# Kernel tuning notes

Measured on AMD Instinct MI355X. Metric: run time of the kernel, lower is better.

The kernel has to match this reference:

```python
import jax, jax.numpy as jnp
import numpy as np

B, CIN, N, K, G, COUT = 8, 128, 2048, 16, 4, 256
NL = COUT // 4          # nl_channels = int(0.25*out_channels) = 64
L = COUT - NL           # l_channels = 192
CL = L // G             # 48 per local head
CNL = NL // G           # 16 per non-local head


def setup_inputs() -> dict:
    key = jax.random.key(0)
    ks = jax.random.split(key, 16)
    s = 0.05
    r = lambda k_, sh: s * jax.random.normal(k_, sh, jnp.float32)
    return {
        "x": jax.random.normal(ks[0], (B, CIN, N, K), jnp.float32),
        "abs_x": jax.random.normal(ks[1], (B, CIN // 2, N, 1), jnp.float32),
        "points": jax.random.normal(ks[2], (B, 3, N), jnp.float32),
        "Wq": r(ks[3], (L, CIN // 2)),
        "Wk": r(ks[4], (L, CIN // 2)),
        "Wv": r(ks[5], (L, CIN)),
        "Wnq": r(ks[6], (NL, CIN // 2)),
        "Wnk": r(ks[7], (NL, CIN // 2)),
        "Wnv1": r(ks[8], (NL, CIN // 2)),
        "Wnv2": r(ks[9], (NL, CIN // 2)),
        "pe_w1": r(ks[10], (3, L)),
        "pe_b1": jnp.zeros((L,), jnp.float32),
        "pe_w2": r(ks[11], (L, L)),
        "pe_b2": jnp.zeros((L,), jnp.float32),
        "npe_w1": r(ks[12], (G, 3, CNL)),
        "npe_b1": jnp.zeros((G, CNL), jnp.float32),
        "npe_w2": r(ks[13], (G, CNL, CNL)),
        "npe_b2": jnp.zeros((G, CNL), jnp.float32),
        "idx": jax.random.randint(ks[14], (B, 1, N, K), 0, N, dtype=jnp.int32),
    }


def _forward(x, abs_x, points, Wq, Wk, Wv, Wnq, Wnk, Wnv1, Wnv2,
             pe_w1, pe_b1, pe_w2, pe_b2, npe_w1, npe_b1, npe_w2, npe_b2, idx):
    b, c, n, k = x.shape
    half = c // 2
    idx_sq = idx[:, 0]                                   # (b,n,k)

    # ---- 1. Local attention over kNN neighbors ----
    lq = jnp.einsum('oc,bcns->bons', Wq, abs_x).reshape(b, G, CL, n, 1)
    lk = jnp.einsum('oc,bcnk->bonk', Wk, x[:, half:] + x[:, :half]).reshape(b, G, CL, n, k)
    lv = jnp.einsum('oc,bcnk->bonk', Wv, x).reshape(b, G, CL, n, k)

    # absolute positional encoding (select_neighbors -> carte MLP)
    nbr = jax.vmap(lambda p, i: p[:, i])(points, idx_sq)  # (b,3,n,k)
    rel = nbr - nbr[..., 0:1]                             # subtract first neighbor
    h = jax.nn.relu(jnp.einsum('bcnk,cd->bnkd', rel, pe_w1) + pe_b1)
    pe = (jnp.einsum('bnkd,de->bnke', h, pe_w2) + pe_b2).transpose(0, 3, 1, 2)
    lk = lk + pe.reshape(b, G, CL, n, k)

    att = jax.nn.softmax((lq * lk).sum(2), axis=-1)       # (b,G,n,k)
    local_feature = jnp.einsum('bgnk,bgcnk->bgcn', att, lv).reshape(b, L, n, 1)

    # ---- scatter-based sparse attention centrality + top-k node selection ----
    idx_flat = idx_sq.reshape(b, n * k)
    att_flat = att.reshape(b, G, n * k)

    def scat(a_g, i):  # a_g: (G, n*k), i: (n*k,)
        return jax.vmap(lambda a: jnp.zeros((n,), a.dtype).at[i].add(a))(a_g)

    cent = jax.vmap(scat)(att_flat, idx_flat)             # (b,G,n)
    vals, inds = jax.lax.top_k(cent, k)                   # (b,G,k)

    # ---- 2. Non-local MHA over selected nodes ----
    a2 = abs_x[..., 0]                                    # (b,half,n)
    nq = jnp.einsum('oc,bcn->bon', Wnq, a2).reshape(b, G, CNL, n)
    nk_ = jnp.einsum('oc,bcn->bon', Wnk, a2).reshape(b, G, CNL, n)
    nv1 = jnp.einsum('oc,bcn->bon', Wnv1, a2).reshape(b, G, CNL, n)
    nv2 = jnp.einsum('oc,bcn->bon', Wnv2, a2).reshape(b, G, CNL, n)

    gi = inds[:, :, None, :]                              # (b,G,1,k)
    nk_sel = jnp.take_along_axis(nk_, gi, axis=3)         # (b,G,CNL,k)
    nv2j = jnp.take_along_axis(nv2, gi, axis=3)           # (b,G,CNL,k)

    # per-group non-local positional encoding (constant over n by construction)
    sel = jnp.take_along_axis(jnp.broadcast_to(points[:, None], (b, G, 3, n)), gi, axis=3)  # (b,G,3,k)
    rel_nl = sel - sel[..., 0:1]
    h2 = jax.nn.relu(jnp.einsum('bgck,gcd->bgkd', rel_nl, npe_w1) + npe_b1[None, :, None, :])
    pe_nl = (jnp.einsum('bgkd,gde->bgke', h2, npe_w2) + npe_b2[None, :, None, :]).transpose(0, 1, 3, 2)  # (b,G,CNL,k)

    att_nl = jax.nn.softmax(jnp.einsum('bgcn,bgck->bgnk', nq, nk_sel + pe_nl), axis=-1)
    # value[b,g,c,n,k] = nv1[...,n] - nv2[...,n] + nv2j[...,k], gated by tanh(centrality)
    w = att_nl * jnp.tanh(vals)[:, :, None, :]            # (b,G,n,k)
    s = w.sum(-1)                                         # (b,G,n)
    nl_feature = (nv1 - nv2) * s[:, :, None, :] + jnp.einsum('bgnk,bgck->bgcn', w, nv2j)
    nl_feature = nl_feature.reshape(b, NL, n, 1)

    return jnp.concatenate([local_feature, nl_feature], axis=1)  # (b,COUT,n,1)


def reference(x, abs_x, points, Wq, Wk, Wv, Wnq, Wnk, Wnv1, Wnv2,
              pe_w1, pe_b1, pe_w2, pe_b2, npe_w1, npe_b1, npe_w2, npe_b2, idx):
    return _forward(x, abs_x, points, Wq, Wk, Wv, Wnq, Wnk, Wnv1, Wnv2,
                    pe_w1, pe_b1, pe_w2, pe_b2, npe_w1, npe_b1, npe_w2, npe_b2, idx)
```

## Files before the change

kernel.cpp:

```cpp
#include <hip/hip_runtime.h>
#include <cstddef>

constexpr int NN = 2048;
constexpr int GG = 4;

__global__ __launch_bounds__(256) void prep_q(const float* __restrict__ Wq,
                                              const float* __restrict__ Wk,
                                              const float* __restrict__ pe_w2,
                                              float* __restrict__ Qbuf) {
    const int g = blockIdx.x >> 6, c2 = blockIdx.x & 63;
    const int row = threadIdx.x;
    float acc = 0.f;
    if (row < 64) {
        for (int j = 0; j < 48; ++j) {
            const int o = g * 48 + j;
            acc = fmaf(Wk[o * 64 + row], Wq[o * 64 + c2], acc);
        }
    } else {
        const int d = row - 64;
        for (int j = 0; j < 48; ++j) {
            const int o = g * 48 + j;
            acc = fmaf(pe_w2[(size_t)d * 192 + o], Wq[o * 64 + c2], acc);
        }
    }
    Qbuf[((size_t)(g * 64 + c2) << 8) + row] = acc;
}

__global__ __launch_bounds__(256, 3) void local_v8(
    const float* __restrict__ x, const float* __restrict__ abs_x,
    const float* __restrict__ points, const float* __restrict__ Wv,
    const float* __restrict__ pe_w1, const float* __restrict__ pe_b1,
    const int* __restrict__ idx, const float* __restrict__ Qbuf,
    float* __restrict__ out, float* __restrict__ cent)
{
    const int bn = blockIdx.x;
    const int b  = bn >> 8;
    const int n0 = (bn & 255) << 3;
    const int tid = threadIdx.x;

    __shared__ int   sidx[128];
    __shared__ float sa2[64][8];
    __shared__ __align__(16) float s_big[4224];
    __shared__ float spart[128][9];
    __shared__ float s_small[544];

    float* sq   = s_big;
    float* sw2  = s_big;
    float* sxw  = s_big;
    float* spts = s_small;
    float* satt = s_small;

    if (tid < 128) sidx[tid] = idx[((size_t)b * NN + n0) * 16 + tid];
    for (int i = tid; i < 512; i += 256) {
        int c = i >> 3, nl = i & 7;
        sa2[c][nl] = abs_x[((size_t)b * 64 + c) * NN + n0 + nl];
    }
    __syncthreads();

    for (int i = tid; i < 384; i += 256) {
        int c3 = i >> 7, r = i & 127;
        spts[(c3 * 8 + (r >> 4)) * 16 + (r & 15)] =
            points[((size_t)b * 3 + c3) * NN + sidx[r]];
    }
    {
        const int g = tid >> 6, row = tid & 63;
        const float* qb = Qbuf + (((size_t)g * 64) << 8) + row;
        float a0 = 0.f, a1 = 0.f, a2v = 0.f, a3 = 0.f,
              a4 = 0.f, a5 = 0.f, a6 = 0.f, a7 = 0.f;
        for (int c2 = 0; c2 < 64; c2 += 8) {
            float qv[8];
            #pragma unroll
            for (int j = 0; j < 8; ++j) qv[j] = qb[(c2 + j) << 8];
            #pragma unroll
            for (int j = 0; j < 8; ++j) {
                const float4 v0 = *(const float4*)&sa2[c2 + j][0];
                const float4 v1 = *(const float4*)&sa2[c2 + j][4];
                a0 = fmaf(qv[j], v0.x, a0); a1 = fmaf(qv[j], v0.y, a1);
                a2v = fmaf(qv[j], v0.z, a2v); a3 = fmaf(qv[j], v0.w, a3);
                a4 = fmaf(qv[j], v1.x, a4); a5 = fmaf(qv[j], v1.y, a5);
                a6 = fmaf(qv[j], v1.z, a6); a7 = fmaf(qv[j], v1.w, a7);
            }
        }
        const int base = (g << 3) * 65 + row;
        sq[base + 0 * 65] = a0; sq[base + 1 * 65] = a1;
        sq[base + 2 * 65] = a2v; sq[base + 3 * 65] = a3;
        sq[base + 4 * 65] = a4; sq[base + 5 * 65] = a5;
        sq[base + 6 * 65] = a6; sq[base + 7 * 65] = a7;
    }
    __syncthreads();

    const int col = tid & 127, dh = tid >> 7;
    const int nlc = col >> 4, kkc = col & 15;

    {
        const float* xp = x + (((size_t)(b * 128 + dh * 32) * NN) + n0 + nlc) * 16 + kkc;
        const size_t cstr = (size_t)NN * 16;
        const float* q0 = &sq[((0 << 3) + nlc) * 65 + dh * 32];
        const float* q1 = &sq[((1 << 3) + nlc) * 65 + dh * 32];
        const float* q2 = &sq[((2 << 3) + nlc) * 65 + dh * 32];
        const float* q3 = &sq[((3 << 3) + nlc) * 65 + dh * 32];
        float a0 = 0.f, a1 = 0.f, a2v = 0.f, a3 = 0.f;
        for (int i0 = 0; i0 < 32; i0 += 8) {
            float lo[8], hi[8];
            #pragma unroll
            for (int j = 0; j < 8; ++j) {
                lo[j] = xp[(size_t)(i0 + j) * cstr];
                hi[j] = xp[(size_t)(i0 + j + 64) * cstr];
            }
            #pragma unroll
            for (int j = 0; j < 8; ++j) {
                const float xs = lo[j] + hi[j];
                a0 = fmaf(q0[i0 + j], xs, a0);
                a1 = fmaf(q1[i0 + j], xs, a1);
                a2v = fmaf(q2[i0 + j], xs, a2v);
                a3 = fmaf(q3[i0 + j], xs, a3);
            }
        }
        spart[col][dh * 4 + 0] = a0; spart[col][dh * 4 + 1] = a1;
        spart[col][dh * 4 + 2] = a2v; spart[col][dh * 4 + 3] = a3;
    }

    float4 xpre[16];
    #pragma unroll
    for (int t = 0; t < 4; ++t) {
        const int i2 = t * 256 + tid;
        const int c = i2 >> 3, nl = i2 & 7;
        const float* xp4 = x + (((size_t)(b * 128 + c) * NN) + n0 + nl) * 16;
        xpre[t * 4 + 0] = *(const float4*)(xp4);
        xpre[t * 4 + 1] = *(const float4*)(xp4 + 4);
        xpre[t * 4 + 2] = *(const float4*)(xp4 + 8);
        xpre[t * 4 + 3] = *(const float4*)(xp4 + 12);
    }
    __syncthreads();

    const float r0 = spts[(0 * 8 + nlc) * 16 + kkc] - spts[(0 * 8 + nlc) * 16];
    const float r1 = spts[(1 * 8 + nlc) * 16 + kkc] - spts[(1 * 8 + nlc) * 16];
    const float r2 = spts[(2 * 8 + nlc) * 16 + kkc] - spts[(2 * 8 + nlc) * 16];
    #pragma unroll
    for (int p = 0; p < 2; ++p) {
        if (tid < 192) {
            const int d = tid;
            float w00=0.f,w01=0.f,w02=0.f,w03=0.f,w04=0.f,w05=0.f,w06=0.f,w07=0.f;
            float w10=0.f,w11=0.f,w12=0.f,w13=0.f,w14=0.f,w15=0.f,w16=0.f,w17=0.f;
            const float* qb0 = Qbuf + (((size_t)(2 * p + 0) * 64) << 8) + 64 + d;
            const float* qb1 = Qbuf + (((size_t)(2 * p + 1) * 64) << 8) + 64 + d;
            for (int c2 = 0; c2 < 64; c2 += 4) {
                float qv0[4], qv1[4];
                #pragma unroll
                for (int j = 0; j < 4; ++j) {
                    qv0[j] = qb0[(c2 + j) << 8];
                    qv1[j] = qb1[(c2 + j) << 8];
                }
                #pragma unroll
                for (int j = 0; j < 4; ++j) {
                    const float4 v0 = *(const float4*)&sa2[c2 + j][0];
                    const float4 v1 = *(const float4*)&sa2[c2 + j][4];
                    w00 = fmaf(qv0[j], v0.x, w00); w01 = fmaf(qv0[j], v0.y, w01);
                    w02 = fmaf(qv0[j], v0.z, w02); w03 = fmaf(qv0[j], v0.w, w03);
                    w04 = fmaf(qv0[j], v1.x, w04); w05 = fmaf(qv0[j], v1.y, w05);
                    w06 = fmaf(qv0[j], v1.z, w06); w07 = fmaf(qv0[j], v1.w, w07);
                    w10 = fmaf(qv1[j], v0.x, w10); w11 = fmaf(qv1[j], v0.y, w11);
                    w12 = fmaf(qv1[j], v0.z, w12); w13 = fmaf(qv1[j], v0.w, w13);
                    w14 = fmaf(qv1[j], v1.x, w14); w15 = fmaf(qv1[j], v1.y, w15);
                    w16 = fmaf(qv1[j], v1.z, w16); w17 = fmaf(qv1[j], v1.w, w17);
                }
            }
            sw2[(0 * 8 + 0) * 196 + d] = w00; sw2[(0 * 8 + 1) * 196 + d] = w01;
            sw2[(0 * 8 + 2) * 196 + d] = w02; sw2[(0 * 8 + 3) * 196 + d] = w03;
            sw2[(0 * 8 + 4) * 196 + d] = w04; sw2[(0 * 8 + 5) * 196 + d] = w05;
            sw2[(0 * 8 + 6) * 196 + d] = w06; sw2[(0 * 8 + 7) * 196 + d] = w07;
            sw2[(1 * 8 + 0) * 196 + d] = w10; sw2[(1 * 8 + 1) * 196 + d] = w11;
            sw2[(1 * 8 + 2) * 196 + d] = w12; sw2[(1 * 8 + 3) * 196 + d] = w13;
            sw2[(1 * 8 + 4) * 196 + d] = w14; sw2[(1 * 8 + 5) * 196 + d] = w15;
            sw2[(1 * 8 + 6) * 196 + d] = w16; sw2[(1 * 8 + 7) * 196 + d] = w17;
        }
        __syncthreads();
        {
            float pB0 = 0.f, pB1 = 0.f;
            const float* w0 = &sw2[(0 * 8 + nlc) * 196];
            const float* w1 = &sw2[(1 * 8 + nlc) * 196];
            const int d0 = dh * 96;
            #pragma unroll 2
            for (int d = d0; d < d0 + 96; d += 4) {
                const float4 w1a = *(const float4*)&pe_w1[d];
                const float4 w1b = *(const float4*)&pe_w1[192 + d];
                const float4 w1c = *(const float4*)&pe_w1[384 + d];
                const float4 bb  = *(const float4*)&pe_b1[d];
                const float h0 = fmaxf(fmaf(r0, w1a.x, fmaf(r1, w1b.x, fmaf(r2, w1c.x, bb.x))), 0.f);
                const float h1 = fmaxf(fmaf(r0, w1a.y, fmaf(r1, w1b.y, fmaf(r2, w1c.y, bb.y))), 0.f);
                const float h2 = fmaxf(fmaf(r0, w1a.z, fmaf(r1, w1b.z, fmaf(r2, w1c.z, bb.z))), 0.f);
                const float h3 = fmaxf(fmaf(r0, w1a.w, fmaf(r1, w1b.w, fmaf(r2, w1c.w, bb.w))), 0.f);
                const float4 wa = *(const float4*)&w0[d];
                const float4 wb = *(const float4*)&w1[d];
                pB0 = fmaf(h0, wa.x, fmaf(h1, wa.y, fmaf(h2, wa.z, fmaf(h3, wa.w, pB0))));
                pB1 = fmaf(h0, wb.x, fmaf(h1, wb.y, fmaf(h2, wb.z, fmaf(h3, wb.w, pB1))));
            }
            spart[col][dh * 4 + 2 * p + 0] += pB0;
            spart[col][dh * 4 + 2 * p + 1] += pB1;
        }
        __syncthreads();
    }

    if (tid < 32) {
        const int g = tid >> 3, nl = tid & 7;
        float lg[16], m = -1e30f;
        #pragma unroll
        for (int kk = 0; kk < 16; ++kk) {
            const int cc = nl * 16 + kk;
            lg[kk] = spart[cc][g] + spart[cc][4 + g];
            m = fmaxf(m, lg[kk]);
        }
        float s = 0.f;
        #pragma unroll
        for (int kk = 0; kk < 16; ++kk) { lg[kk] = __expf(lg[kk] - m); s += lg[kk]; }
        const float inv = 1.f / s;
        #pragma unroll
        for (int kk = 0; kk < 16; ++kk) satt[nl * 68 + g * 16 + kk] = lg[kk] * inv;
    }
    __syncthreads();

    #pragma unroll
    for (int t = 0; t < 4; ++t) {
        const int i2 = t * 256 + tid;
        const int c = i2 >> 3, nl = i2 & 7;
        const float4 x0 = xpre[t * 4 + 0];
        const float4 x1 = xpre[t * 4 + 1];
        const float4 x2 = xpre[t * 4 + 2];
        const float4 x3 = xpre[t * 4 + 3];
        const float* at = &satt[nl * 68];
        #pragma unroll
        for (int g = 0; g < 4; ++g) {
            const float* a = at + g * 16;
            float v = 0.f;
            v = fmaf(x0.x, a[0],  v); v = fmaf(x0.y, a[1],  v);
            v = fmaf(x0.z, a[2],  v); v = fmaf(x0.w, a[3],  v);
            v = fmaf(x1.x, a[4],  v); v = fmaf(x1.y, a[5],  v);
            v = fmaf(x1.z, a[6],  v); v = fmaf(x1.w, a[7],  v);
            v = fmaf(x2.x, a[8],  v); v = fmaf(x2.y, a[9],  v);
            v = fmaf(x2.z, a[10], v); v = fmaf(x2.w, a[11], v);
            v = fmaf(x3.x, a[12], v); v = fmaf(x3.y, a[13], v);
            v = fmaf(x3.z, a[14], v); v = fmaf(x3.w, a[15], v);
            sxw[((g << 3) + nl) * 132 + c] = v;
        }
    }
    __syncthreads();

    #pragma unroll
    for (int rep = 0; rep < 6; ++rep) {
        const int i = rep * 256 + tid;
        const int o = i >> 3, nl = i & 7;
        const int g = o / 48;
        const float* wv  = Wv + (size_t)o * 128;
        const float* xwp = &sxw[((g << 3) + nl) * 132];
        float a = 0.f;
        #pragma unroll 8
        for (int c = 0; c < 128; c += 4) {
            const float4 w4  = *(const float4*)(wv + c);
            const float4 xw4 = *(const float4*)(xwp + c);
            a = fmaf(w4.x, xw4.x, fmaf(w4.y, xw4.y, fmaf(w4.z, xw4.z, fmaf(w4.w, xw4.w, a))));
        }
        out[(((size_t)b << 8) + o) * NN + n0 + nl] = a;
    }

    if (tid < 32) {
        const int g = tid >> 3, nl = tid & 7;
        #pragma unroll
        for (int kk = 0; kk < 16; ++kk)
            atomicAdd(&cent[((size_t)(b * GG + g) << 11) + sidx[nl * 16 + kk]],
                      satt[nl * 68 + g * 16 + kk]);
    }
}

__global__ __launch_bounds__(512) void topk_prep_kernel(
    const float* __restrict__ abs_x, const float* __restrict__ points,
    const float* __restrict__ Wnk, const float* __restrict__ Wnv2,
    const float* __restrict__ npe_w1, const float* __restrict__ npe_b1,
    const float* __restrict__ npe_w2, const float* __restrict__ npe_b2,
    const float* __restrict__ cent,
    float* __restrict__ nkpe, float* __restrict__ nv2j, float* __restrict__ tanhv)
{
    const int bg  = blockIdx.x;
    const int b   = bg >> 2, g = bg & 3;
    const int tid = threadIdx.x;
    const int wave = tid >> 6, lane = tid & 63;
    __shared__ float sc[2048];
    __shared__ float cval[128]; __shared__ int cidx[128];
    __shared__ float svals[16]; __shared__ int sinds[16];
    __shared__ float srel[3][16];
    __shared__ float sh2[16][16];

    for (int i = tid; i < 2048; i += 512) sc[i] = cent[((size_t)bg << 11) + i];
    __syncthreads();

    {
        float v[4]; int ix[4];
        #pragma unroll
        for (int j = 0; j < 4; ++j) {
            const int i = wave * 256 + j * 64 + lane;
            v[j] = sc[i]; ix[j] = i;
        }
        for (int t = 0; t < 16; ++t) {
            float bv = v[0]; int bi = ix[0];
            #pragma unroll
            for (int j = 1; j < 4; ++j)
                if (v[j] > bv || (v[j] == bv && ix[j] < bi)) { bv = v[j]; bi = ix[j]; }
            float wv_ = bv; int wi_ = bi;
            #pragma unroll
            for (int off = 1; off < 64; off <<= 1) {
                const float ov = __shfl_xor(wv_, off, 64);
                const int   oi = __shfl_xor(wi_, off, 64);
                if (ov > wv_ || (ov == wv_ && oi < wi_)) { wv_ = ov; wi_ = oi; }
            }
            #pragma unroll
            for (int j = 0; j < 4; ++j)
                if (ix[j] == wi_) { v[j] = -1e30f; ix[j] = 1 << 30; }
            if (lane == 0) { cval[wave * 16 + t] = wv_; cidx[wave * 16 + t] = wi_; }
        }
    }
    __syncthreads();

    if (wave == 0) {
        float m0 = cval[lane], m1 = cval[64 + lane];
        int   j0 = cidx[lane], j1 = cidx[64 + lane];
        for (int t = 0; t < 16; ++t) {
            float bv; int bi;
            if (m0 > m1 || (m0 == m1 && j0 < j1)) { bv = m0; bi = j0; }
            else { bv = m1; bi = j1; }
            float wv_ = bv; int wi_ = bi;
            #pragma unroll
            for (int off = 1; off < 64; off <<= 1) {
                const float ov = __shfl_xor(wv_, off, 64);
                const int   oi = __shfl_xor(wi_, off, 64);
                if (ov > wv_ || (ov == wv_ && oi < wi_)) { wv_ = ov; wi_ = oi; }
            }
            if (j0 == wi_) { m0 = -1e30f; j0 = 1 << 30; }
            if (j1 == wi_) { m1 = -1e30f; j1 = 1 << 30; }
            if (lane == 0) { svals[t] = wv_; sinds[t] = wi_; }
        }
    }
    __syncthreads();

    if (tid < 48) {
        int c = tid >> 4, j = tid & 15;
        srel[c][j] = points[((size_t)b * 3 + c) * NN + sinds[j]]
                   - points[((size_t)b * 3 + c) * NN + sinds[0]];
    }
    __syncthreads();
    if (tid < 256) {
        int j = tid >> 4, d = tid & 15;
        float a = npe_b1[g * 16 + d];
        #pragma unroll
        for (int c = 0; c < 3; ++c) a = fmaf(srel[c][j], npe_w1[((g * 3 + c) << 4) + d], a);
        sh2[j][d] = fmaxf(a, 0.f);
    }
    __syncthreads();
    if (tid < 256) {
        int c = tid >> 4, j = tid & 15;
        float a = npe_b2[g * 16 + c];
        #pragma unroll
        for (int d = 0; d < 16; ++d) a = fmaf(sh2[j][d], npe_w2[((g * 16 + d) << 4) + c], a);
        float nk = 0.f, nv = 0.f;
        const int colj = sinds[j];
        const float* a2  = abs_x + (size_t)b * 64 * NN + colj;
        const float* wkr = Wnk  + ((size_t)(g * 16 + c) << 6);
        const float* wvr = Wnv2 + ((size_t)(g * 16 + c) << 6);
        for (int ci = 0; ci < 64; ++ci) {
            float av = a2[(size_t)ci * NN];
            nk = fmaf(wkr[ci], av, nk);
            nv = fmaf(wvr[ci], av, nv);
        }
        nkpe[((size_t)bg << 8) + (c << 4) + j] = nk + a;
        nv2j[((size_t)bg << 8) + (c << 4) + j] = nv;
    }
    if (tid < 16) tanhv[(bg << 4) + tid] = tanhf(svals[tid]);
}

__global__ __launch_bounds__(256) void nonlocal_kernel(
    const float* __restrict__ abs_x,
    const float* __restrict__ Wnq, const float* __restrict__ Wnv1, const float* __restrict__ Wnv2,
    const float* __restrict__ nkpe, const float* __restrict__ nv2j, const float* __restrict__ tanhv,
    float* __restrict__ out)
{
    const int blk = blockIdx.x;
    const int b   = blk >> 5;
    const int n0  = (blk & 31) << 6;
    const int tid = threadIdx.x;
    const int nl  = tid & 63;
    const int g   = tid >> 6;

    __shared__ float sa2[64][64];
    __shared__ float snkpe[4][16][16];
    __shared__ float snv2j[4][16][16];
    __shared__ float stanh[4][16];

    for (int i = tid; i < 64 * 64; i += 256) {
        int ci = i >> 6, c2 = i & 63;
        sa2[ci][c2] = abs_x[((size_t)b * 64 + ci) * NN + n0 + c2];
    }
    for (int i = tid; i < 1024; i += 256) {
        ((float*)snkpe)[i] = nkpe[((size_t)b << 10) + i];
        ((float*)snv2j)[i] = nv2j[((size_t)b << 10) + i];
    }
    if (tid < 64) ((float*)stanh)[tid] = tanhv[(b << 6) + tid];
    __syncthreads();

    float nq[16], nv1[16], nv2[16];
    #pragma unroll
    for (int c = 0; c < 16; ++c) { nq[c] = 0.f; nv1[c] = 0.f; nv2[c] = 0.f; }
    const float* wq  = Wnq  + (size_t)(g << 4) * 64;
    const float* wv1 = Wnv1 + (size_t)(g << 4) * 64;
    const float* wv2 = Wnv2 + (size_t)(g << 4) * 64;
    for (int ci = 0; ci < 64; ++ci) {
        const float a = sa2[ci][nl];
        #pragma unroll
        for (int c = 0; c < 16; ++c) {
            nq[c]  = fmaf(wq [(c << 6) + ci], a, nq[c]);
            nv1[c] = fmaf(wv1[(c << 6) + ci], a, nv1[c]);
            nv2[c] = fmaf(wv2[(c << 6) + ci], a, nv2[c]);
        }
    }

    float lg[16];
    #pragma unroll
    for (int j = 0; j < 16; ++j) {
        float a = 0.f;
        #pragma unroll
        for (int c = 0; c < 16; ++c) a = fmaf(nq[c], snkpe[g][c][j], a);
        lg[j] = a;
    }
    float m = lg[0];
    #pragma unroll
    for (int j = 1; j < 16; ++j) m = fmaxf(m, lg[j]);
    float s = 0.f;
    float w[16];
    #pragma unroll
    for (int j = 0; j < 16; ++j) { w[j] = __expf(lg[j] - m); s += w[j]; }
    const float inv = 1.f / s;
    float ws = 0.f;
    #pragma unroll
    for (int j = 0; j < 16; ++j) { w[j] = w[j] * inv * stanh[g][j]; ws += w[j]; }
    #pragma unroll
    for (int c = 0; c < 16; ++c) {
        float v = (nv1[c] - nv2[c]) * ws;
        #pragma unroll
        for (int j = 0; j < 16; ++j) v = fmaf(w[j], snv2j[g][c][j], v);
        out[(((size_t)b << 8) + 192 + (g << 4) + c) * NN + n0 + nl] = v;
    }
}

extern "C" void kernel_launch(void* const* d_in, const int* in_sizes, int n_in,
                              void* d_out, int out_size, void* d_ws, size_t ws_size,
                              hipStream_t stream)
{
    (void)in_sizes; (void)n_in; (void)out_size; (void)ws_size;
    const float* x      = (const float*)d_in[0];
    const float* abs_x  = (const float*)d_in[1];
    const float* points = (const float*)d_in[2];
    const float* Wq     = (const float*)d_in[3];
    const float* Wk     = (const float*)d_in[4];
    const float* Wv     = (const float*)d_in[5];
    const float* Wnq    = (const float*)d_in[6];
    const float* Wnk    = (const float*)d_in[7];
    const float* Wnv1   = (const float*)d_in[8];
    const float* Wnv2   = (const float*)d_in[9];
    const float* pe_w1  = (const float*)d_in[10];
    const float* pe_b1  = (const float*)d_in[11];
    const float* pe_w2  = (const float*)d_in[12];
    const float* npe_w1 = (const float*)d_in[14];
    const float* npe_b1 = (const float*)d_in[15];
    const float* npe_w2 = (const float*)d_in[16];
    const float* npe_b2 = (const float*)d_in[17];
    const int*   idx    = (const int*)d_in[18];
    float* out = (float*)d_out;

    float* cent  = (float*)d_ws;
    float* Qbuf  = cent + 65536;
    float* nkpeW = Qbuf + 65536;
    float* nv2jW = nkpeW + 8192;
    float* tanhW = nv2jW + 8192;

    hipMemsetAsync(cent, 0, (size_t)65536 * sizeof(float), stream);
    prep_q<<<256, 256, 0, stream>>>(Wq, Wk, pe_w2, Qbuf);
    local_v8<<<2048, 256, 0, stream>>>(x, abs_x, points, Wv, pe_w1, pe_b1,
                                       idx, Qbuf, out, cent);
    topk_prep_kernel<<<32, 512, 0, stream>>>(abs_x, points, Wnk, Wnv2,
                                             npe_w1, npe_b1, npe_w2, npe_b2,
                                             cent, nkpeW, nv2jW, tanhW);
    nonlocal_kernel<<<8 * 32, 256, 0, stream>>>(abs_x, Wnq, Wnv1, Wnv2,
                                                nkpeW, nv2jW, tanhW, out);
}
```

Measured before the change: 251.6 us.

## Split per-point query projection into separate kernel and drop x register prefetch

Moves the abs_x×Qbuf projection (both the key-side and positional-encoding-side weights) out of the local attention kernel into a new qw_kernel that writes a per-point 1024-float buffer to workspace. The local kernel then loads these precomputed rows instead of recomputing them, and reloads x values at use instead of holding them in registers. This trades in-kernel FMA work and register pressure for a large global-memory write and read of the intermediate buffer plus an extra launch.

```diff
diff --git a/kernel.cpp b/kernel.cpp
--- a/kernel.cpp
+++ b/kernel.cpp
@@ -26,11 +26,51 @@
     Qbuf[((size_t)(g * 64 + c2) << 8) + row] = acc;
 }
 
-__global__ __launch_bounds__(256, 3) void local_v8(
-    const float* __restrict__ x, const float* __restrict__ abs_x,
-    const float* __restrict__ points, const float* __restrict__ Wv,
+__global__ __launch_bounds__(256, 4) void qw_kernel(
+    const float* __restrict__ abs_x, const float* __restrict__ Qbuf,
+    float* __restrict__ QW)
+{
+    const int bt = blockIdx.x;
+    const int b  = bt >> 8;
+    const int n0 = (bt & 255) << 3;
+    const int tid = threadIdx.x;
+    __shared__ float sa2[64][8];
+    for (int i = tid; i < 512; i += 256) {
+        int c = i >> 3, nl = i & 7;
+        sa2[c][nl] = abs_x[((size_t)b * 64 + c) * NN + n0 + nl];
+    }
+    __syncthreads();
+    #pragma unroll
+    for (int g = 0; g < 4; ++g) {
+        const float* qb = Qbuf + ((size_t)g << 14) + tid;
+        float a0 = 0.f, a1 = 0.f, a2v = 0.f, a3 = 0.f, a4 = 0.f, a5 = 0.f, a6 = 0.f, a7 = 0.f;
+        for (int c2 = 0; c2 < 64; c2 += 4) {
+            float qv[4];
+            #pragma unroll
+            for (int j = 0; j < 4; ++j) qv[j] = qb[(c2 + j) << 8];
+            #pragma unroll
+            for (int j = 0; j < 4; ++j) {
+                const float4 v0 = *(const float4*)&sa2[c2 + j][0];
+                const float4 v1 = *(const float4*)&sa2[c2 + j][4];
+                a0 = fmaf(qv[j], v0.x, a0); a1 = fmaf(qv[j], v0.y, a1);
+                a2v = fmaf(qv[j], v0.z, a2v); a3 = fmaf(qv[j], v0.w, a3);
+                a4 = fmaf(qv[j], v1.x, a4); a5 = fmaf(qv[j], v1.y, a5);
+                a6 = fmaf(qv[j], v1.z, a6); a7 = fmaf(qv[j], v1.w, a7);
+            }
+        }
+        float* op = QW + (((size_t)(b * NN + n0)) << 10) + (g << 8) + tid;
+        op[0] = a0;
+        op[(size_t)1 << 10] = a1; op[(size_t)2 << 10] = a2v; op[(size_t)3 << 10] = a3;
+        op[(size_t)4 << 10] = a4; op[(size_t)5 << 10] = a5;
+        op[(size_t)6 << 10] = a6; op[(size_t)7 << 10] = a7;
+    }
+}
+
+__global__ __launch_bounds__(256, 3) void local_v9(
+    const float* __restrict__ x, const float* __restrict__ points,
+    const float* __restrict__ Wv,
     const float* __restrict__ pe_w1, const float* __restrict__ pe_b1,
-    const int* __restrict__ idx, const float* __restrict__ Qbuf,
+    const int* __restrict__ idx, const float* __restrict__ QW,
     float* __restrict__ out, float* __restrict__ cent)
 {
     const int bn = blockIdx.x;
@@ -39,7 +79,6 @@
     const int tid = threadIdx.x;
 
     __shared__ int   sidx[128];
-    __shared__ float sa2[64][8];
     __shared__ __align__(16) float s_big[4224];
     __shared__ float spart[128][9];
     __shared__ float s_small[544];
@@ -51,9 +90,14 @@
     float* satt = s_small;
 
     if (tid < 128) sidx[tid] = idx[((size_t)b * NN + n0) * 16 + tid];
-    for (int i = tid; i < 512; i += 256) {
-        int c = i >> 3, nl = i & 7;
-        sa2[c][nl] = abs_x[((size_t)b * 64 + c) * NN + n0 + nl];
+    {
+        const float* qsrc = QW + ((size_t)(b * NN + n0) << 10);
+        #pragma unroll
+        for (int t = 0; t < 8; ++t) {
+            const int i = t * 256 + tid;
+            const int g = i >> 9, nl = (i >> 6) & 7, c2 = i & 63;
+            sq[((g << 3) + nl) * 65 + c2] = qsrc[((size_t)nl << 10) + (g << 8) + c2];
+        }
     }
     __syncthreads();
 
@@ -62,32 +106,6 @@
         spts[(c3 * 8 + (r >> 4)) * 16 + (r & 15)] =
             points[((size_t)b * 3 + c3) * NN + sidx[r]];
     }
-    {
-        const int g = tid >> 6, row = tid & 63;
-        const float* qb = Qbuf + (((size_t)g * 64) << 8) + row;
-        float a0 = 0.f, a1 = 0.f, a2v = 0.f, a3 = 0.f,
-              a4 = 0.f, a5 = 0.f, a6 = 0.f, a7 = 0.f;
-        for (int c2 = 0; c2 < 64; c2 += 8) {
-            float qv[8];
-            #pragma unroll
-            for (int j = 0; j < 8; ++j) qv[j] = qb[(c2 + j) << 8];
-            #pragma unroll
-            for (int j = 0; j < 8; ++j) {
-                const float4 v0 = *(const float4*)&sa2[c2 + j][0];
-                const float4 v1 = *(const float4*)&sa2[c2 + j][4];
-                a0 = fmaf(qv[j], v0.x, a0); a1 = fmaf(qv[j], v0.y, a1);
-                a2v = fmaf(qv[j], v0.z, a2v); a3 = fmaf(qv[j], v0.w, a3);
-                a4 = fmaf(qv[j], v1.x, a4); a5 = fmaf(qv[j], v1.y, a5);
-                a6 = fmaf(qv[j], v1.z, a6); a7 = fmaf(qv[j], v1.w, a7);
-            }
-        }
-        const int base = (g << 3) * 65 + row;
-        sq[base + 0 * 65] = a0; sq[base + 1 * 65] = a1;
-        sq[base + 2 * 65] = a2v; sq[base + 3 * 65] = a3;
-        sq[base + 4 * 65] = a4; sq[base + 5 * 65] = a5;
-        sq[base + 6 * 65] = a6; sq[base + 7 * 65] = a7;
-    }
-    __syncthreads();
 
     const int col = tid & 127, dh = tid >> 7;
     const int nlc = col >> 4, kkc = col & 15;
@@ -119,18 +137,6 @@
         spart[col][dh * 4 + 0] = a0; spart[col][dh * 4 + 1] = a1;
         spart[col][dh * 4 + 2] = a2v; spart[col][dh * 4 + 3] = a3;
     }
-
-    float4 xpre[16];
-    #pragma unroll
-    for (int t = 0; t < 4; ++t) {
-        const int i2 = t * 256 + tid;
-        const int c = i2 >> 3, nl = i2 & 7;
-        const float* xp4 = x + (((size_t)(b * 128 + c) * NN) + n0 + nl) * 16;
-        xpre[t * 4 + 0] = *(const float4*)(xp4);
-        xpre[t * 4 + 1] = *(const float4*)(xp4 + 4);
-        xpre[t * 4 + 2] = *(const float4*)(xp4 + 8);
-        xpre[t * 4 + 3] = *(const float4*)(xp4 + 12);
-    }
     __syncthreads();
 
     const float r0 = spts[(0 * 8 + nlc) * 16 + kkc] - spts[(0 * 8 + nlc) * 16];
@@ -138,41 +144,14 @@
     const float r2 = spts[(2 * 8 + nlc) * 16 + kkc] - spts[(2 * 8 + nlc) * 16];
     #pragma unroll
     for (int p = 0; p < 2; ++p) {
-        if (tid < 192) {
-            const int d = tid;
-            float w00=0.f,w01=0.f,w02=0.f,w03=0.f,w04=0.f,w05=0.f,w06=0.f,w07=0.f;
-            float w10=0.f,w11=0.f,w12=0.f,w13=0.f,w14=0.f,w15=0.f,w16=0.f,w17=0.f;
-            const float* qb0 = Qbuf + (((size_t)(2 * p + 0) * 64) << 8) + 64 + d;
-            const float* qb1 = Qbuf + (((size_t)(2 * p + 1) * 64) << 8) + 64 + d;
-            for (int c2 = 0; c2 < 64; c2 += 4) {
-                float qv0[4], qv1[4];
-                #pragma unroll
-                for (int j = 0; j < 4; ++j) {
-                    qv0[j] = qb0[(c2 + j) << 8];
-                    qv1[j] = qb1[(c2 + j) << 8];
-                }
-                #pragma unroll
-                for (int j = 0; j < 4; ++j) {
-                    const float4 v0 = *(const float4*)&sa2[c2 + j][0];
-                    const float4 v1 = *(const float4*)&sa2[c2 + j][4];
-                    w00 = fmaf(qv0[j], v0.x, w00); w01 = fmaf(qv0[j], v0.y, w01);
-                    w02 = fmaf(qv0[j], v0.z, w02); w03 = fmaf(qv0[j], v0.w, w03);
-                    w04 = fmaf(qv0[j], v1.x, w04); w05 = fmaf(qv0[j], v1.y, w05);
-                    w06 = fmaf(qv0[j], v1.z, w06); w07 = fmaf(qv0[j], v1.w, w07);
-                    w10 = fmaf(qv1[j], v0.x, w10); w11 = fmaf(qv1[j], v0.y, w11);
-                    w12 = fmaf(qv1[j], v0.z, w12); w13 = fmaf(qv1[j], v0.w, w13);
-                    w14 = fmaf(qv1[j], v1.x, w14); w15 = fmaf(qv1[j], v1.y, w15);
-                    w16 = fmaf(qv1[j], v1.z, w16); w17 = fmaf(qv1[j], v1.w, w17);
-                }
-            }
-            sw2[(0 * 8 + 0) * 196 + d] = w00; sw2[(0 * 8 + 1) * 196 + d] = w01;
-            sw2[(0 * 8 + 2) * 196 + d] = w02; sw2[(0 * 8 + 3) * 196 + d] = w03;
-            sw2[(0 * 8 + 4) * 196 + d] = w04; sw2[(0 * 8 + 5) * 196 + d] = w05;
-            sw2[(0 * 8 + 6) * 196 + d] = w06; sw2[(0 * 8 + 7) * 196 + d] = w07;
-            sw2[(1 * 8 + 0) * 196 + d] = w10; sw2[(1 * 8 + 1) * 196 + d] = w11;
-            sw2[(1 * 8 + 2) * 196 + d] = w12; sw2[(1 * 8 + 3) * 196 + d] = w13;
-            sw2[(1 * 8 + 4) * 196 + d] = w14; sw2[(1 * 8 + 5) * 196 + d] = w15;
-            sw2[(1 * 8 + 6) * 196 + d] = w16; sw2[(1 * 8 + 7) * 196 + d] = w17;
+        #pragma unroll
+        for (int k = 0; k < 3; ++k) {
+            const int q = k * 256 + tid;
+            const int row = q / 48, dq = q - row * 48;
+            const int gg = row >> 3, nl = row & 7;
+            const float4 v = *(const float4*)(QW + ((size_t)(b * NN + n0 + nl) << 10)
+                                              + ((2 * p + gg) << 8) + 64 + dq * 4);
+            *(float4*)&sw2[row * 196 + dq * 4] = v;
         }
         __syncthreads();
         {
@@ -223,10 +202,11 @@
     for (int t = 0; t < 4; ++t) {
         const int i2 = t * 256 + tid;
         const int c = i2 >> 3, nl = i2 & 7;
-        const float4 x0 = xpre[t * 4 + 0];
-        const float4 x1 = xpre[t * 4 + 1];
-        const float4 x2 = xpre[t * 4 + 2];
-        const float4 x3 = xpre[t * 4 + 3];
+        const float* xp4 = x + (((size_t)(b * 128 + c) * NN) + n0 + nl) * 16;
+        const float4 x0 = *(const float4*)(xp4);
+        const float4 x1 = *(const float4*)(xp4 + 4);
+        const float4 x2 = *(const float4*)(xp4 + 8);
+        const float4 x3 = *(const float4*)(xp4 + 12);
         const float* at = &satt[nl * 68];
         #pragma unroll
         for (int g = 0; g < 4; ++g) {
@@ -452,7 +432,7 @@
                               void* d_out, int out_size, void* d_ws, size_t ws_size,
                               hipStream_t stream)
 {
-    (void)in_sizes; (void)n_in; (void)out_size; (void)ws_size;
+    (void)in_sizes; (void)n_in; (void)out_size;
     const float* x      = (const float*)d_in[0];
     const float* abs_x  = (const float*)d_in[1];
     const float* points = (const float*)d_in[2];
@@ -478,11 +458,14 @@
     float* nkpeW = Qbuf + 65536;
     float* nv2jW = nkpeW + 8192;
     float* tanhW = nv2jW + 8192;
+    float* QW    = tanhW + 512;
+    (void)ws_size;
 
     hipMemsetAsync(cent, 0, (size_t)65536 * sizeof(float), stream);
     prep_q<<<256, 256, 0, stream>>>(Wq, Wk, pe_w2, Qbuf);
-    local_v8<<<2048, 256, 0, stream>>>(x, abs_x, points, Wv, pe_w1, pe_b1,
-                                       idx, Qbuf, out, cent);
+    qw_kernel<<<2048, 256, 0, stream>>>(abs_x, Qbuf, QW);
+    local_v9<<<2048, 256, 0, stream>>>(x, points, Wv, pe_w1, pe_b1,
+                                       idx, QW, out, cent);
     topk_prep_kernel<<<32, 512, 0, stream>>>(abs_x, points, Wnk, Wnv2,
                                              npe_w1, npe_b1, npe_w2, npe_b2,
                                              cent, nkpeW, nv2jW, tanhW);
```

After: 311.7 us. 1.24x slower.
